# Optimization experiments

Measured on AMD Instinct MI355X. Metric: run time of the kernel, lower is better.

## Reference

```python
import jax, jax.numpy as jnp
import numpy as np

B = 2097152
SCALE, SHIFT = 1.5, 0.2
EPS = 1e-5
H, DK = 2, 2  # num_heads, d_k (embed_dim=4)


def _lin(x, w, b):
    return x @ w.T + b


def _ln(x, w, b):
    mu = jnp.mean(x, -1, keepdims=True)
    var = jnp.mean((x - mu) ** 2, -1, keepdims=True)
    return (x - mu) / jnp.sqrt(var + EPS) * w + b


def setup_inputs() -> dict:
    key = jax.random.key(0)
    ks = iter(jax.random.split(key, 40))
    def W(o, i):
        return jax.random.normal(next(ks), (o, i), jnp.float32) * (1.0 / np.sqrt(i))
    def Bv(o):
        return jax.random.normal(next(ks), (o,), jnp.float32) * 0.05
    d = {
        'inputs': jax.random.normal(next(ks), (B, 8), jnp.float32),
        'fm_w': W(16, 8), 'fm_b': Bv(16),
        'c1_w': W(16, 16), 'c1_b': Bv(16),
        'p1_w': W(12, 16), 'p1_b': Bv(12),
        'c2_w': W(8, 12), 'c2_b': Bv(8),
        'p2_w': W(4, 8), 'p2_b': Bv(4),
        'c3_w': W(4, 4), 'c3_b': Bv(4),
        'q_w': W(4, 4), 'q_b': Bv(4),
        'k_w': W(4, 4), 'k_b': Bv(4),
        'v_w': W(4, 4), 'v_b': Bv(4),
        'o_w': W(4, 4), 'o_b': Bv(4),
        'ln1_w': jnp.ones(4), 'ln1_b': jnp.zeros(4),
        'ln2_w': jnp.ones(4), 'ln2_b': jnp.zeros(4),
        'ffn1_w': W(8, 4), 'ffn1_b': Bv(8),
        'ffn2_w': W(4, 8), 'ffn2_b': Bv(4),
        'fs_w': W(4, 4), 'fs_b': Bv(4),
        'head_w': W(1, 4), 'head_b': Bv(1),
    }
    return d


def reference(inputs, fm_w, fm_b, c1_w, c1_b, p1_w, p1_b, c2_w, c2_b, p2_w, p2_b,
              c3_w, c3_b, q_w, q_b, k_w, k_b, v_w, v_b, o_w, o_b,
              ln1_w, ln1_b, ln2_w, ln2_b, ffn1_w, ffn1_b, ffn2_w, ffn2_b,
              fs_w, fs_b, head_w, head_b):
    x = jnp.tanh(_lin(inputs, fm_w, fm_b))
    x = jnp.tanh(_lin(x, c1_w, c1_b))
    x = jnp.tanh(_lin(x, p1_w, p1_b))
    x = jnp.tanh(_lin(x, c2_w, c2_b))
    x = jnp.tanh(_lin(x, p2_w, p2_b))
    x = jnp.tanh(_lin(x, c3_w, c3_b))
    # transformer block with seq_len = 1 (eval mode -> dropout identity)
    xs = x[:, None, :]  # [B, 1, 4]
    b, s, _ = xs.shape
    q = _lin(xs, q_w, q_b).reshape(b, s, H, DK).transpose(0, 2, 1, 3)
    k = _lin(xs, k_w, k_b).reshape(b, s, H, DK).transpose(0, 2, 1, 3)
    v = _lin(xs, v_w, v_b).reshape(b, s, H, DK).transpose(0, 2, 1, 3)
    scores = jnp.einsum('bhsd,bhtd->bhst', q, k) / np.sqrt(DK).astype(np.float32)
    attn = jax.nn.softmax(scores, axis=-1)
    out = jnp.einsum('bhst,bhtd->bhsd', attn, v).transpose(0, 2, 1, 3).reshape(b, s, H * DK)
    attn_out = _lin(out, o_w, o_b)
    xs = _ln(xs + attn_out, ln1_w, ln1_b)
    ffn = _lin(jax.nn.relu(_lin(xs, ffn1_w, ffn1_b)), ffn2_w, ffn2_b)
    xs = _ln(xs + ffn, ln2_w, ln2_b)
    x = xs[:, 0, :]
    x = jnp.tanh(_lin(x, fs_w, fs_b)) * SCALE + SHIFT
    return jax.nn.sigmoid(_lin(x, head_w, head_b))
```

## Files before the change

kernel.cpp:

```cpp
#include <hip/hip_runtime.h>

#define BS 256

typedef float f32x2 __attribute__((ext_vector_type(2)));

__device__ __forceinline__ f32x2 splat2(float v) {
  f32x2 r; r[0] = v; r[1] = v; return r;
}
__device__ __forceinline__ f32x2 pkfma(float w, f32x2 x, f32x2 a) {
  return __builtin_elementwise_fma(splat2(w), x, a);
}

__device__ __forceinline__ f32x2 fast_tanh2(f32x2 x) {
  f32x2 z = x * 2.8853900817779268f;
  f32x2 t;
  t[0] = __builtin_amdgcn_exp2f(z[0]);
  t[1] = __builtin_amdgcn_exp2f(z[1]);
  f32x2 tp1 = t + 1.0f;
  f32x2 r;
  r[0] = __builtin_amdgcn_rcpf(tp1[0]);
  r[1] = __builtin_amdgcn_rcpf(tp1[1]);
  return __builtin_elementwise_fma(splat2(-2.0f), r, splat2(1.0f));
}
__device__ __forceinline__ f32x2 fast_sigmoid2(f32x2 x) {
  f32x2 z = x * -1.4426950408889634f;
  f32x2 t;
  t[0] = __builtin_amdgcn_exp2f(z[0]);
  t[1] = __builtin_amdgcn_exp2f(z[1]);
  f32x2 tp1 = t + 1.0f;
  f32x2 r;
  r[0] = __builtin_amdgcn_rcpf(tp1[0]);
  r[1] = __builtin_amdgcn_rcpf(tp1[1]);
  return r;
}
__device__ __forceinline__ f32x2 relu2(f32x2 x) {
  f32x2 r;
  r[0] = fmaxf(x[0], 0.0f);
  r[1] = fmaxf(x[1], 0.0f);
  return r;
}

#define D4(W, B, O, p0, p1, p2, p3)                                            \
  pkfma((W)[(O)*4 + 0], p0,                                                    \
  pkfma((W)[(O)*4 + 1], p1,                                                    \
  pkfma((W)[(O)*4 + 2], p2,                                                    \
  pkfma((W)[(O)*4 + 3], p3, splat2((B)[O])))))

#define D8(W, B, O, p0, p1, p2, p3, p4, p5, p6, p7)                            \
  pkfma((W)[(O)*8 + 0], p0,                                                    \
  pkfma((W)[(O)*8 + 1], p1,                                                    \
  pkfma((W)[(O)*8 + 2], p2,                                                    \
  pkfma((W)[(O)*8 + 3], p3,                                                    \
  pkfma((W)[(O)*8 + 4], p4,                                                    \
  pkfma((W)[(O)*8 + 5], p5,                                                    \
  pkfma((W)[(O)*8 + 6], p6,                                                    \
  pkfma((W)[(O)*8 + 7], p7, splat2((B)[O])))))))))

#define D12(W, B, O, p0, p1, p2, p3, p4, p5, p6, p7, p8, p9, pa, pb)           \
  pkfma((W)[(O)*12 + 0], p0,                                                   \
  pkfma((W)[(O)*12 + 1], p1,                                                   \
  pkfma((W)[(O)*12 + 2], p2,                                                   \
  pkfma((W)[(O)*12 + 3], p3,                                                   \
  pkfma((W)[(O)*12 + 4], p4,                                                   \
  pkfma((W)[(O)*12 + 5], p5,                                                   \
  pkfma((W)[(O)*12 + 6], p6,                                                   \
  pkfma((W)[(O)*12 + 7], p7,                                                   \
  pkfma((W)[(O)*12 + 8], p8,                                                   \
  pkfma((W)[(O)*12 + 9], p9,                                                   \
  pkfma((W)[(O)*12 +10], pa,                                                   \
  pkfma((W)[(O)*12 +11], pb, splat2((B)[O])))))))))))))

#define D16(W, B, O, p0, p1, p2, p3, p4, p5, p6, p7, p8, p9, pa, pb, pc, pd, pe, pf) \
  pkfma((W)[(O)*16 + 0], p0,                                                   \
  pkfma((W)[(O)*16 + 1], p1,                                                   \
  pkfma((W)[(O)*16 + 2], p2,                                                   \
  pkfma((W)[(O)*16 + 3], p3,                                                   \
  pkfma((W)[(O)*16 + 4], p4,                                                   \
  pkfma((W)[(O)*16 + 5], p5,                                                   \
  pkfma((W)[(O)*16 + 6], p6,                                                   \
  pkfma((W)[(O)*16 + 7], p7,                                                   \
  pkfma((W)[(O)*16 + 8], p8,                                                   \
  pkfma((W)[(O)*16 + 9], p9,                                                   \
  pkfma((W)[(O)*16 +10], pa,                                                   \
  pkfma((W)[(O)*16 +11], pb,                                                   \
  pkfma((W)[(O)*16 +12], pc,                                                   \
  pkfma((W)[(O)*16 +13], pd,                                                   \
  pkfma((W)[(O)*16 +14], pe,                                                   \
  pkfma((W)[(O)*16 +15], pf, splat2((B)[O])))))))))))))))))

__global__ void __launch_bounds__(BS) qcnn_pk2(
    const float* __restrict__ inp,
    const float* __restrict__ fm_w,  const float* __restrict__ fm_b,
    const float* __restrict__ c1_w,  const float* __restrict__ c1_b,
    const float* __restrict__ p1_w,  const float* __restrict__ p1_b,
    const float* __restrict__ c2_w,  const float* __restrict__ c2_b,
    const float* __restrict__ p2_w,  const float* __restrict__ p2_b,
    const float* __restrict__ c3_w,  const float* __restrict__ c3_b,
    const float* __restrict__ v_w,   const float* __restrict__ v_b,
    const float* __restrict__ o_w,   const float* __restrict__ o_b,
    const float* __restrict__ ln1_w, const float* __restrict__ ln1_b,
    const float* __restrict__ ln2_w, const float* __restrict__ ln2_b,
    const float* __restrict__ ffn1_w, const float* __restrict__ ffn1_b,
    const float* __restrict__ ffn2_w, const float* __restrict__ ffn2_b,
    const float* __restrict__ fs_w,  const float* __restrict__ fs_b,
    const float* __restrict__ head_w, const float* __restrict__ head_b,
    float* __restrict__ out, long long nrows) {
  const long long gid = (long long)blockIdx.x * BS + threadIdx.x;
  const long long row0 = gid * 2;
  if (row0 >= nrows) return;
  const bool ok1 = (row0 + 1) < nrows;

  const float4* __restrict__ in4 = reinterpret_cast<const float4*>(inp);
  float4 r0lo = in4[gid * 4 + 0];
  float4 r0hi = in4[gid * 4 + 1];
  float4 r1lo, r1hi;
  if (ok1) {
    r1lo = in4[gid * 4 + 2];
    r1hi = in4[gid * 4 + 3];
  } else {
    r1lo = float4{0.f, 0.f, 0.f, 0.f};
    r1hi = float4{0.f, 0.f, 0.f, 0.f};
  }
  f32x2 x0 = {r0lo.x, r1lo.x}, x1 = {r0lo.y, r1lo.y};
  f32x2 x2 = {r0lo.z, r1lo.z}, x3 = {r0lo.w, r1lo.w};
  f32x2 x4 = {r0hi.x, r1hi.x}, x5 = {r0hi.y, r1hi.y};
  f32x2 x6 = {r0hi.z, r1hi.z}, x7 = {r0hi.w, r1hi.w};

#define LFM(O) fast_tanh2(D8(fm_w, fm_b, O, x0, x1, x2, x3, x4, x5, x6, x7))
  f32x2 a0 = LFM(0),  a1 = LFM(1),  a2 = LFM(2),  a3 = LFM(3);
  f32x2 a4 = LFM(4),  a5 = LFM(5),  a6 = LFM(6),  a7 = LFM(7);
  f32x2 a8 = LFM(8),  a9 = LFM(9),  aa = LFM(10), ab = LFM(11);
  f32x2 ac = LFM(12), ad = LFM(13), ae = LFM(14), af = LFM(15);

#define LC1(O) fast_tanh2(D16(c1_w, c1_b, O, a0,a1,a2,a3,a4,a5,a6,a7,a8,a9,aa,ab,ac,ad,ae,af))
  f32x2 b0 = LC1(0),  b1 = LC1(1),  b2 = LC1(2),  b3 = LC1(3);
  f32x2 b4 = LC1(4),  b5 = LC1(5),  b6 = LC1(6),  b7 = LC1(7);
  f32x2 b8 = LC1(8),  b9 = LC1(9),  ba = LC1(10), bb = LC1(11);
  f32x2 bc = LC1(12), bd = LC1(13), be = LC1(14), bf = LC1(15);

#define LP1(O) fast_tanh2(D16(p1_w, p1_b, O, b0,b1,b2,b3,b4,b5,b6,b7,b8,b9,ba,bb,bc,bd,be,bf))
  f32x2 c0 = LP1(0),  c1 = LP1(1),  c2 = LP1(2),  c3 = LP1(3);
  f32x2 c4 = LP1(4),  c5 = LP1(5),  c6 = LP1(6),  c7 = LP1(7);
  f32x2 c8 = LP1(8),  c9 = LP1(9),  ca = LP1(10), cb = LP1(11);

#define LC2(O) fast_tanh2(D12(c2_w, c2_b, O, c0,c1,c2,c3,c4,c5,c6,c7,c8,c9,ca,cb))
  f32x2 d0 = LC2(0), d1 = LC2(1), d2 = LC2(2), d3 = LC2(3);
  f32x2 d4 = LC2(4), d5 = LC2(5), d6 = LC2(6), d7 = LC2(7);

#define LP2(O) fast_tanh2(D8(p2_w, p2_b, O, d0, d1, d2, d3, d4, d5, d6, d7))
  f32x2 e0 = LP2(0), e1 = LP2(1), e2 = LP2(2), e3 = LP2(3);

  f32x2 s0 = fast_tanh2(D4(c3_w, c3_b, 0, e0, e1, e2, e3));
  f32x2 s1 = fast_tanh2(D4(c3_w, c3_b, 1, e0, e1, e2, e3));
  f32x2 s2 = fast_tanh2(D4(c3_w, c3_b, 2, e0, e1, e2, e3));
  f32x2 s3 = fast_tanh2(D4(c3_w, c3_b, 3, e0, e1, e2, e3));

  f32x2 v0 = D4(v_w, v_b, 0, s0, s1, s2, s3);
  f32x2 v1 = D4(v_w, v_b, 1, s0, s1, s2, s3);
  f32x2 v2 = D4(v_w, v_b, 2, s0, s1, s2, s3);
  f32x2 v3 = D4(v_w, v_b, 3, s0, s1, s2, s3);
  f32x2 o0 = D4(o_w, o_b, 0, v0, v1, v2, v3);
  f32x2 o1 = D4(o_w, o_b, 1, v0, v1, v2, v3);
  f32x2 o2 = D4(o_w, o_b, 2, v0, v1, v2, v3);
  f32x2 o3 = D4(o_w, o_b, 3, v0, v1, v2, v3);

  f32x2 t0 = s0 + o0, t1 = s1 + o1, t2 = s2 + o2, t3 = s3 + o3;
  f32x2 mu = (t0 + t1 + t2 + t3) * 0.25f;
  f32x2 q0 = t0 - mu, q1 = t1 - mu, q2 = t2 - mu, q3 = t3 - mu;
  f32x2 var = (q0 * q0 + q1 * q1 + q2 * q2 + q3 * q3) * 0.25f + 1e-5f;
  f32x2 inv;
  inv[0] = __builtin_amdgcn_rsqf(var[0]);
  inv[1] = __builtin_amdgcn_rsqf(var[1]);
  f32x2 n0 = q0 * inv * ln1_w[0] + ln1_b[0];
  f32x2 n1 = q1 * inv * ln1_w[1] + ln1_b[1];
  f32x2 n2 = q2 * inv * ln1_w[2] + ln1_b[2];
  f32x2 n3 = q3 * inv * ln1_w[3] + ln1_b[3];

#define LF1(O) relu2(D4(ffn1_w, ffn1_b, O, n0, n1, n2, n3))
  f32x2 f0 = LF1(0), f1 = LF1(1), f2 = LF1(2), f3 = LF1(3);
  f32x2 f4 = LF1(4), f5 = LF1(5), f6 = LF1(6), f7 = LF1(7);
  f32x2 g0 = D8(ffn2_w, ffn2_b, 0, f0, f1, f2, f3, f4, f5, f6, f7);
  f32x2 g1 = D8(ffn2_w, ffn2_b, 1, f0, f1, f2, f3, f4, f5, f6, f7);
  f32x2 g2 = D8(ffn2_w, ffn2_b, 2, f0, f1, f2, f3, f4, f5, f6, f7);
  f32x2 g3 = D8(ffn2_w, ffn2_b, 3, f0, f1, f2, f3, f4, f5, f6, f7);

  f32x2 u0 = n0 + g0, u1 = n1 + g1, u2 = n2 + g2, u3 = n3 + g3;
  f32x2 mu2 = (u0 + u1 + u2 + u3) * 0.25f;
  f32x2 w0 = u0 - mu2, w1 = u1 - mu2, w2 = u2 - mu2, w3 = u3 - mu2;
  f32x2 var2 = (w0 * w0 + w1 * w1 + w2 * w2 + w3 * w3) * 0.25f + 1e-5f;
  f32x2 inv2;
  inv2[0] = __builtin_amdgcn_rsqf(var2[0]);
  inv2[1] = __builtin_amdgcn_rsqf(var2[1]);
  f32x2 m0 = w0 * inv2 * ln2_w[0] + ln2_b[0];
  f32x2 m1 = w1 * inv2 * ln2_w[1] + ln2_b[1];
  f32x2 m2 = w2 * inv2 * ln2_w[2] + ln2_b[2];
  f32x2 m3 = w3 * inv2 * ln2_w[3] + ln2_b[3];

  f32x2 h0 = fast_tanh2(D4(fs_w, fs_b, 0, m0, m1, m2, m3)) * 1.5f + 0.2f;
  f32x2 h1 = fast_tanh2(D4(fs_w, fs_b, 1, m0, m1, m2, m3)) * 1.5f + 0.2f;
  f32x2 h2 = fast_tanh2(D4(fs_w, fs_b, 2, m0, m1, m2, m3)) * 1.5f + 0.2f;
  f32x2 h3 = fast_tanh2(D4(fs_w, fs_b, 3, m0, m1, m2, m3)) * 1.5f + 0.2f;
  f32x2 y = pkfma(head_w[3], h3,
            pkfma(head_w[2], h2,
            pkfma(head_w[1], h1,
            pkfma(head_w[0], h0, splat2(head_b[0])))));
  y = fast_sigmoid2(y);

  if (ok1) {
    reinterpret_cast<float2*>(out)[gid] = make_float2(y[0], y[1]);
  } else {
    out[row0] = y[0];
  }
}

extern "C" void kernel_launch(void* const* d_in, const int* in_sizes, int n_in,
                              void* d_out, int out_size, void* d_ws, size_t ws_size,
                              hipStream_t stream) {
  const float* inp = (const float*)d_in[0];
  long long nrows = (long long)in_sizes[0] / 8;
  long long nthreads = (nrows + 1) / 2;
  dim3 grid((unsigned)((nthreads + BS - 1) / BS)), block(BS);
  qcnn_pk2<<<grid, block, 0, stream>>>(
      inp,
      (const float*)d_in[1],  (const float*)d_in[2],
      (const float*)d_in[3],  (const float*)d_in[4],
      (const float*)d_in[5],  (const float*)d_in[6],
      (const float*)d_in[7],  (const float*)d_in[8],
      (const float*)d_in[9],  (const float*)d_in[10],
      (const float*)d_in[11], (const float*)d_in[12],
      (const float*)d_in[17], (const float*)d_in[18],
      (const float*)d_in[19], (const float*)d_in[20],
      (const float*)d_in[21], (const float*)d_in[22],
      (const float*)d_in[23], (const float*)d_in[24],
      (const float*)d_in[25], (const float*)d_in[26],
      (const float*)d_in[27], (const float*)d_in[28],
      (const float*)d_in[29], (const float*)d_in[30],
      (const float*)d_in[31], (const float*)d_in[32],
      (float*)d_out, nrows);
}
```

Baseline: 59.44 us.

## Replace exp/rcp tanh with Pade rational and process four rows per thread

Swaps the transcendental-unit tanh (exp2 plus rcp) for a clamped [7/6] Pade rational approximation whose reciprocal is computed by a magic-constant guess refined with Newton steps, so the work runs entirely as packed FMA-able VALU ops. Each thread now handles four rows instead of two, giving more packed-math parallelism and float4 output stores. The cost is more ALU instructions per tanh, higher register pressure from the wider vectors, and half as many threads, which may reduce occupancy and latency hiding.

```diff
diff --git a/kernel.cpp b/kernel.cpp
--- a/kernel.cpp
+++ b/kernel.cpp
@@ -2,49 +2,62 @@
 
 #define BS 256
 
-typedef float f32x2 __attribute__((ext_vector_type(2)));
-
-__device__ __forceinline__ f32x2 splat2(float v) {
-  f32x2 r; r[0] = v; r[1] = v; return r;
-}
-__device__ __forceinline__ f32x2 pkfma(float w, f32x2 x, f32x2 a) {
-  return __builtin_elementwise_fma(splat2(w), x, a);
-}
-
-__device__ __forceinline__ f32x2 fast_tanh2(f32x2 x) {
-  f32x2 z = x * 2.8853900817779268f;
-  f32x2 t;
-  t[0] = __builtin_amdgcn_exp2f(z[0]);
-  t[1] = __builtin_amdgcn_exp2f(z[1]);
-  f32x2 tp1 = t + 1.0f;
-  f32x2 r;
-  r[0] = __builtin_amdgcn_rcpf(tp1[0]);
-  r[1] = __builtin_amdgcn_rcpf(tp1[1]);
-  return __builtin_elementwise_fma(splat2(-2.0f), r, splat2(1.0f));
-}
-__device__ __forceinline__ f32x2 fast_sigmoid2(f32x2 x) {
-  f32x2 z = x * -1.4426950408889634f;
-  f32x2 t;
-  t[0] = __builtin_amdgcn_exp2f(z[0]);
-  t[1] = __builtin_amdgcn_exp2f(z[1]);
-  f32x2 tp1 = t + 1.0f;
-  f32x2 r;
-  r[0] = __builtin_amdgcn_rcpf(tp1[0]);
-  r[1] = __builtin_amdgcn_rcpf(tp1[1]);
+typedef float f32x4 __attribute__((ext_vector_type(4)));
+typedef unsigned int u32x4 __attribute__((ext_vector_type(4)));
+
+__device__ __forceinline__ f32x4 splat4(float v) {
+  f32x4 r; r[0] = v; r[1] = v; r[2] = v; r[3] = v; return r;
+}
+__device__ __forceinline__ f32x4 pkfma(float w, f32x4 x, f32x4 a) {
+  return __builtin_elementwise_fma(splat4(w), x, a);
+}
+
+__device__ __forceinline__ f32x4 tanh_pade(f32x4 x) {
+  f32x4 a;
+#pragma unroll
+  for (int e = 0; e < 4; ++e) a[e] = __builtin_amdgcn_fmed3f(x[e], -6.0f, 6.0f);
+  f32x4 t = a * a;
+  f32x4 n = t + 378.0f;
+  n = __builtin_elementwise_fma(n, t, splat4(17325.0f));
+  n = __builtin_elementwise_fma(n, t, splat4(135135.0f));
+  n = n * a;
+  f32x4 d = __builtin_elementwise_fma(t, splat4(28.0f), splat4(3150.0f));
+  d = __builtin_elementwise_fma(d, t, splat4(62370.0f));
+  d = __builtin_elementwise_fma(d, t, splat4(135135.0f));
+  u32x4 bi = __builtin_bit_cast(u32x4, d);
+  u32x4 yi = 0x7EF311C3u - bi;
+  f32x4 y = __builtin_bit_cast(f32x4, yi);
+#pragma unroll
+  for (int it = 0; it < 3; ++it) {
+    f32x4 u = __builtin_elementwise_fma(-d, y, splat4(2.0f));
+    y = y * u;
+  }
+  f32x4 r = n * y;
+#pragma unroll
+  for (int e = 0; e < 4; ++e) r[e] = __builtin_amdgcn_fmed3f(r[e], -1.0f, 1.0f);
   return r;
 }
-__device__ __forceinline__ f32x2 relu2(f32x2 x) {
-  f32x2 r;
-  r[0] = fmaxf(x[0], 0.0f);
-  r[1] = fmaxf(x[1], 0.0f);
+
+__device__ __forceinline__ f32x4 fast_sigmoid4(f32x4 x) {
+  f32x4 z = x * -1.4426950408889634f;
+  f32x4 t;
+#pragma unroll
+  for (int e = 0; e < 4; ++e) t[e] = __builtin_amdgcn_exp2f(z[e]);
+  f32x4 tp1 = t + 1.0f;
+  f32x4 r;
+#pragma unroll
+  for (int e = 0; e < 4; ++e) r[e] = __builtin_amdgcn_rcpf(tp1[e]);
   return r;
+}
+__device__ __forceinline__ f32x4 relu4(f32x4 x) {
+  return __builtin_elementwise_max(x, splat4(0.0f));
 }
 
 #define D4(W, B, O, p0, p1, p2, p3)                                            \
   pkfma((W)[(O)*4 + 0], p0,                                                    \
   pkfma((W)[(O)*4 + 1], p1,                                                    \
   pkfma((W)[(O)*4 + 2], p2,                                                    \
-  pkfma((W)[(O)*4 + 3], p3, splat2((B)[O])))))
+  pkfma((W)[(O)*4 + 3], p3, splat4((B)[O])))))
 
 #define D8(W, B, O, p0, p1, p2, p3, p4, p5, p6, p7)                            \
   pkfma((W)[(O)*8 + 0], p0,                                                    \
@@ -54,7 +67,7 @@
   pkfma((W)[(O)*8 + 4], p4,                                                    \
   pkfma((W)[(O)*8 + 5], p5,                                                    \
   pkfma((W)[(O)*8 + 6], p6,                                                    \
-  pkfma((W)[(O)*8 + 7], p7, splat2((B)[O])))))))))
+  pkfma((W)[(O)*8 + 7], p7, splat4((B)[O])))))))))
 
 #define D12(W, B, O, p0, p1, p2, p3, p4, p5, p6, p7, p8, p9, pa, pb)           \
   pkfma((W)[(O)*12 + 0], p0,                                                   \
@@ -68,7 +81,7 @@
   pkfma((W)[(O)*12 + 8], p8,                                                   \
   pkfma((W)[(O)*12 + 9], p9,                                                   \
   pkfma((W)[(O)*12 +10], pa,                                                   \
-  pkfma((W)[(O)*12 +11], pb, splat2((B)[O])))))))))))))
+  pkfma((W)[(O)*12 +11], pb, splat4((B)[O])))))))))))))
 
 #define D16(W, B, O, p0, p1, p2, p3, p4, p5, p6, p7, p8, p9, pa, pb, pc, pd, pe, pf) \
   pkfma((W)[(O)*16 + 0], p0,                                                   \
@@ -86,9 +99,9 @@
   pkfma((W)[(O)*16 +12], pc,                                                   \
   pkfma((W)[(O)*16 +13], pd,                                                   \
   pkfma((W)[(O)*16 +14], pe,                                                   \
-  pkfma((W)[(O)*16 +15], pf, splat2((B)[O])))))))))))))))))
-
-__global__ void __launch_bounds__(BS) qcnn_pk2(
+  pkfma((W)[(O)*16 +15], pf, splat4((B)[O])))))))))))))))))
+
+__global__ void __launch_bounds__(BS) qcnn_pade(
     const float* __restrict__ inp,
     const float* __restrict__ fm_w,  const float* __restrict__ fm_b,
     const float* __restrict__ c1_w,  const float* __restrict__ c1_b,
@@ -106,110 +119,114 @@
     const float* __restrict__ head_w, const float* __restrict__ head_b,
     float* __restrict__ out, long long nrows) {
   const long long gid = (long long)blockIdx.x * BS + threadIdx.x;
-  const long long row0 = gid * 2;
+  const long long row0 = gid * 4;
   if (row0 >= nrows) return;
-  const bool ok1 = (row0 + 1) < nrows;
+  const long long rA = row0;
+  const long long rB = (row0 + 1 < nrows) ? row0 + 1 : nrows - 1;
+  const long long rC = (row0 + 2 < nrows) ? row0 + 2 : nrows - 1;
+  const long long rD = (row0 + 3 < nrows) ? row0 + 3 : nrows - 1;
 
   const float4* __restrict__ in4 = reinterpret_cast<const float4*>(inp);
-  float4 r0lo = in4[gid * 4 + 0];
-  float4 r0hi = in4[gid * 4 + 1];
-  float4 r1lo, r1hi;
-  if (ok1) {
-    r1lo = in4[gid * 4 + 2];
-    r1hi = in4[gid * 4 + 3];
-  } else {
-    r1lo = float4{0.f, 0.f, 0.f, 0.f};
-    r1hi = float4{0.f, 0.f, 0.f, 0.f};
-  }
-  f32x2 x0 = {r0lo.x, r1lo.x}, x1 = {r0lo.y, r1lo.y};
-  f32x2 x2 = {r0lo.z, r1lo.z}, x3 = {r0lo.w, r1lo.w};
-  f32x2 x4 = {r0hi.x, r1hi.x}, x5 = {r0hi.y, r1hi.y};
-  f32x2 x6 = {r0hi.z, r1hi.z}, x7 = {r0hi.w, r1hi.w};
-
-#define LFM(O) fast_tanh2(D8(fm_w, fm_b, O, x0, x1, x2, x3, x4, x5, x6, x7))
-  f32x2 a0 = LFM(0),  a1 = LFM(1),  a2 = LFM(2),  a3 = LFM(3);
-  f32x2 a4 = LFM(4),  a5 = LFM(5),  a6 = LFM(6),  a7 = LFM(7);
-  f32x2 a8 = LFM(8),  a9 = LFM(9),  aa = LFM(10), ab = LFM(11);
-  f32x2 ac = LFM(12), ad = LFM(13), ae = LFM(14), af = LFM(15);
-
-#define LC1(O) fast_tanh2(D16(c1_w, c1_b, O, a0,a1,a2,a3,a4,a5,a6,a7,a8,a9,aa,ab,ac,ad,ae,af))
-  f32x2 b0 = LC1(0),  b1 = LC1(1),  b2 = LC1(2),  b3 = LC1(3);
-  f32x2 b4 = LC1(4),  b5 = LC1(5),  b6 = LC1(6),  b7 = LC1(7);
-  f32x2 b8 = LC1(8),  b9 = LC1(9),  ba = LC1(10), bb = LC1(11);
-  f32x2 bc = LC1(12), bd = LC1(13), be = LC1(14), bf = LC1(15);
-
-#define LP1(O) fast_tanh2(D16(p1_w, p1_b, O, b0,b1,b2,b3,b4,b5,b6,b7,b8,b9,ba,bb,bc,bd,be,bf))
-  f32x2 c0 = LP1(0),  c1 = LP1(1),  c2 = LP1(2),  c3 = LP1(3);
-  f32x2 c4 = LP1(4),  c5 = LP1(5),  c6 = LP1(6),  c7 = LP1(7);
-  f32x2 c8 = LP1(8),  c9 = LP1(9),  ca = LP1(10), cb = LP1(11);
-
-#define LC2(O) fast_tanh2(D12(c2_w, c2_b, O, c0,c1,c2,c3,c4,c5,c6,c7,c8,c9,ca,cb))
-  f32x2 d0 = LC2(0), d1 = LC2(1), d2 = LC2(2), d3 = LC2(3);
-  f32x2 d4 = LC2(4), d5 = LC2(5), d6 = LC2(6), d7 = LC2(7);
-
-#define LP2(O) fast_tanh2(D8(p2_w, p2_b, O, d0, d1, d2, d3, d4, d5, d6, d7))
-  f32x2 e0 = LP2(0), e1 = LP2(1), e2 = LP2(2), e3 = LP2(3);
-
-  f32x2 s0 = fast_tanh2(D4(c3_w, c3_b, 0, e0, e1, e2, e3));
-  f32x2 s1 = fast_tanh2(D4(c3_w, c3_b, 1, e0, e1, e2, e3));
-  f32x2 s2 = fast_tanh2(D4(c3_w, c3_b, 2, e0, e1, e2, e3));
-  f32x2 s3 = fast_tanh2(D4(c3_w, c3_b, 3, e0, e1, e2, e3));
-
-  f32x2 v0 = D4(v_w, v_b, 0, s0, s1, s2, s3);
-  f32x2 v1 = D4(v_w, v_b, 1, s0, s1, s2, s3);
-  f32x2 v2 = D4(v_w, v_b, 2, s0, s1, s2, s3);
-  f32x2 v3 = D4(v_w, v_b, 3, s0, s1, s2, s3);
-  f32x2 o0 = D4(o_w, o_b, 0, v0, v1, v2, v3);
-  f32x2 o1 = D4(o_w, o_b, 1, v0, v1, v2, v3);
-  f32x2 o2 = D4(o_w, o_b, 2, v0, v1, v2, v3);
-  f32x2 o3 = D4(o_w, o_b, 3, v0, v1, v2, v3);
-
-  f32x2 t0 = s0 + o0, t1 = s1 + o1, t2 = s2 + o2, t3 = s3 + o3;
-  f32x2 mu = (t0 + t1 + t2 + t3) * 0.25f;
-  f32x2 q0 = t0 - mu, q1 = t1 - mu, q2 = t2 - mu, q3 = t3 - mu;
-  f32x2 var = (q0 * q0 + q1 * q1 + q2 * q2 + q3 * q3) * 0.25f + 1e-5f;
-  f32x2 inv;
-  inv[0] = __builtin_amdgcn_rsqf(var[0]);
-  inv[1] = __builtin_amdgcn_rsqf(var[1]);
-  f32x2 n0 = q0 * inv * ln1_w[0] + ln1_b[0];
-  f32x2 n1 = q1 * inv * ln1_w[1] + ln1_b[1];
-  f32x2 n2 = q2 * inv * ln1_w[2] + ln1_b[2];
-  f32x2 n3 = q3 * inv * ln1_w[3] + ln1_b[3];
-
-#define LF1(O) relu2(D4(ffn1_w, ffn1_b, O, n0, n1, n2, n3))
-  f32x2 f0 = LF1(0), f1 = LF1(1), f2 = LF1(2), f3 = LF1(3);
-  f32x2 f4 = LF1(4), f5 = LF1(5), f6 = LF1(6), f7 = LF1(7);
-  f32x2 g0 = D8(ffn2_w, ffn2_b, 0, f0, f1, f2, f3, f4, f5, f6, f7);
-  f32x2 g1 = D8(ffn2_w, ffn2_b, 1, f0, f1, f2, f3, f4, f5, f6, f7);
-  f32x2 g2 = D8(ffn2_w, ffn2_b, 2, f0, f1, f2, f3, f4, f5, f6, f7);
-  f32x2 g3 = D8(ffn2_w, ffn2_b, 3, f0, f1, f2, f3, f4, f5, f6, f7);
-
-  f32x2 u0 = n0 + g0, u1 = n1 + g1, u2 = n2 + g2, u3 = n3 + g3;
-  f32x2 mu2 = (u0 + u1 + u2 + u3) * 0.25f;
-  f32x2 w0 = u0 - mu2, w1 = u1 - mu2, w2 = u2 - mu2, w3 = u3 - mu2;
-  f32x2 var2 = (w0 * w0 + w1 * w1 + w2 * w2 + w3 * w3) * 0.25f + 1e-5f;
-  f32x2 inv2;
-  inv2[0] = __builtin_amdgcn_rsqf(var2[0]);
-  inv2[1] = __builtin_amdgcn_rsqf(var2[1]);
-  f32x2 m0 = w0 * inv2 * ln2_w[0] + ln2_b[0];
-  f32x2 m1 = w1 * inv2 * ln2_w[1] + ln2_b[1];
-  f32x2 m2 = w2 * inv2 * ln2_w[2] + ln2_b[2];
-  f32x2 m3 = w3 * inv2 * ln2_w[3] + ln2_b[3];
-
-  f32x2 h0 = fast_tanh2(D4(fs_w, fs_b, 0, m0, m1, m2, m3)) * 1.5f + 0.2f;
-  f32x2 h1 = fast_tanh2(D4(fs_w, fs_b, 1, m0, m1, m2, m3)) * 1.5f + 0.2f;
-  f32x2 h2 = fast_tanh2(D4(fs_w, fs_b, 2, m0, m1, m2, m3)) * 1.5f + 0.2f;
-  f32x2 h3 = fast_tanh2(D4(fs_w, fs_b, 3, m0, m1, m2, m3)) * 1.5f + 0.2f;
-  f32x2 y = pkfma(head_w[3], h3,
+  float4 aLo = in4[rA * 2 + 0], aHi = in4[rA * 2 + 1];
+  float4 bLo = in4[rB * 2 + 0], bHi = in4[rB * 2 + 1];
+  float4 cLo = in4[rC * 2 + 0], cHi = in4[rC * 2 + 1];
+  float4 dLo = in4[rD * 2 + 0], dHi = in4[rD * 2 + 1];
+  f32x4 x0 = {aLo.x, bLo.x, cLo.x, dLo.x};
+  f32x4 x1 = {aLo.y, bLo.y, cLo.y, dLo.y};
+  f32x4 x2 = {aLo.z, bLo.z, cLo.z, dLo.z};
+  f32x4 x3 = {aLo.w, bLo.w, cLo.w, dLo.w};
+  f32x4 x4 = {aHi.x, bHi.x, cHi.x, dHi.x};
+  f32x4 x5 = {aHi.y, bHi.y, cHi.y, dHi.y};
+  f32x4 x6 = {aHi.z, bHi.z, cHi.z, dHi.z};
+  f32x4 x7 = {aHi.w, bHi.w, cHi.w, dHi.w};
+
+#define LFM(O) tanh_pade(D8(fm_w, fm_b, O, x0, x1, x2, x3, x4, x5, x6, x7))
+  f32x4 a0 = LFM(0),  a1 = LFM(1),  a2 = LFM(2),  a3 = LFM(3);
+  f32x4 a4 = LFM(4),  a5 = LFM(5),  a6 = LFM(6),  a7 = LFM(7);
+  f32x4 a8 = LFM(8),  a9 = LFM(9),  aa = LFM(10), ab = LFM(11);
+  f32x4 ac = LFM(12), ad = LFM(13), ae = LFM(14), af = LFM(15);
+
+#define LC1(O) tanh_pade(D16(c1_w, c1_b, O, a0,a1,a2,a3,a4,a5,a6,a7,a8,a9,aa,ab,ac,ad,ae,af))
+  f32x4 b0 = LC1(0),  b1 = LC1(1),  b2 = LC1(2),  b3 = LC1(3);
+  f32x4 b4 = LC1(4),  b5 = LC1(5),  b6 = LC1(6),  b7 = LC1(7);
+  f32x4 b8 = LC1(8),  b9 = LC1(9),  ba = LC1(10), bb = LC1(11);
+  f32x4 bc = LC1(12), bd = LC1(13), be = LC1(14), bf = LC1(15);
+
+#define LP1(O) tanh_pade(D16(p1_w, p1_b, O, b0,b1,b2,b3,b4,b5,b6,b7,b8,b9,ba,bb,bc,bd,be,bf))
+  f32x4 c0 = LP1(0),  c1 = LP1(1),  c2 = LP1(2),  c3 = LP1(3);
+  f32x4 c4 = LP1(4),  c5 = LP1(5),  c6 = LP1(6),  c7 = LP1(7);
+  f32x4 c8 = LP1(8),  c9 = LP1(9),  ca = LP1(10), cb = LP1(11);
+
+#define LC2(O) tanh_pade(D12(c2_w, c2_b, O, c0,c1,c2,c3,c4,c5,c6,c7,c8,c9,ca,cb))
+  f32x4 d0 = LC2(0), d1 = LC2(1), d2 = LC2(2), d3 = LC2(3);
+  f32x4 d4 = LC2(4), d5 = LC2(5), d6 = LC2(6), d7 = LC2(7);
+
+#define LP2(O) tanh_pade(D8(p2_w, p2_b, O, d0, d1, d2, d3, d4, d5, d6, d7))
+  f32x4 e0 = LP2(0), e1 = LP2(1), e2 = LP2(2), e3 = LP2(3);
+
+  f32x4 s0 = tanh_pade(D4(c3_w, c3_b, 0, e0, e1, e2, e3));
+  f32x4 s1 = tanh_pade(D4(c3_w, c3_b, 1, e0, e1, e2, e3));
+  f32x4 s2 = tanh_pade(D4(c3_w, c3_b, 2, e0, e1, e2, e3));
+  f32x4 s3 = tanh_pade(D4(c3_w, c3_b, 3, e0, e1, e2, e3));
+
+  f32x4 v0 = D4(v_w, v_b, 0, s0, s1, s2, s3);
+  f32x4 v1 = D4(v_w, v_b, 1, s0, s1, s2, s3);
+  f32x4 v2 = D4(v_w, v_b, 2, s0, s1, s2, s3);
+  f32x4 v3 = D4(v_w, v_b, 3, s0, s1, s2, s3);
+  f32x4 o0 = D4(o_w, o_b, 0, v0, v1, v2, v3);
+  f32x4 o1 = D4(o_w, o_b, 1, v0, v1, v2, v3);
+  f32x4 o2 = D4(o_w, o_b, 2, v0, v1, v2, v3);
+  f32x4 o3 = D4(o_w, o_b, 3, v0, v1, v2, v3);
+
+  f32x4 t0 = s0 + o0, t1 = s1 + o1, t2 = s2 + o2, t3 = s3 + o3;
+  f32x4 mu = (t0 + t1 + t2 + t3) * 0.25f;
+  f32x4 q0 = t0 - mu, q1 = t1 - mu, q2 = t2 - mu, q3 = t3 - mu;
+  f32x4 var = (q0 * q0 + q1 * q1 + q2 * q2 + q3 * q3) * 0.25f + 1e-5f;
+  f32x4 inv;
+#pragma unroll
+  for (int e = 0; e < 4; ++e) inv[e] = __builtin_amdgcn_rsqf(var[e]);
+  f32x4 n0 = q0 * inv * ln1_w[0] + ln1_b[0];
+  f32x4 n1 = q1 * inv * ln1_w[1] + ln1_b[1];
+  f32x4 n2 = q2 * inv * ln1_w[2] + ln1_b[2];
+  f32x4 n3 = q3 * inv * ln1_w[3] + ln1_b[3];
+
+#define LF1(O) relu4(D4(ffn1_w, ffn1_b, O, n0, n1, n2, n3))
+  f32x4 f0 = LF1(0), f1 = LF1(1), f2 = LF1(2), f3 = LF1(3);
+  f32x4 f4 = LF1(4), f5 = LF1(5), f6 = LF1(6), f7 = LF1(7);
+  f32x4 g0 = D8(ffn2_w, ffn2_b, 0, f0, f1, f2, f3, f4, f5, f6, f7);
+  f32x4 g1 = D8(ffn2_w, ffn2_b, 1, f0, f1, f2, f3, f4, f5, f6, f7);
+  f32x4 g2 = D8(ffn2_w, ffn2_b, 2, f0, f1, f2, f3, f4, f5, f6, f7);
+  f32x4 g3 = D8(ffn2_w, ffn2_b, 3, f0, f1, f2, f3, f4, f5, f6, f7);
+
+  f32x4 u0 = n0 + g0, u1 = n1 + g1, u2 = n2 + g2, u3 = n3 + g3;
+  f32x4 mu2 = (u0 + u1 + u2 + u3) * 0.25f;
+  f32x4 w0 = u0 - mu2, w1 = u1 - mu2, w2 = u2 - mu2, w3 = u3 - mu2;
+  f32x4 var2 = (w0 * w0 + w1 * w1 + w2 * w2 + w3 * w3) * 0.25f + 1e-5f;
+  f32x4 inv2;
+#pragma unroll
+  for (int e = 0; e < 4; ++e) inv2[e] = __builtin_amdgcn_rsqf(var2[e]);
+  f32x4 m0 = w0 * inv2 * ln2_w[0] + ln2_b[0];
+  f32x4 m1 = w1 * inv2 * ln2_w[1] + ln2_b[1];
+  f32x4 m2 = w2 * inv2 * ln2_w[2] + ln2_b[2];
+  f32x4 m3 = w3 * inv2 * ln2_w[3] + ln2_b[3];
+
+  f32x4 h0 = tanh_pade(D4(fs_w, fs_b, 0, m0, m1, m2, m3)) * 1.5f + 0.2f;
+  f32x4 h1 = tanh_pade(D4(fs_w, fs_b, 1, m0, m1, m2, m3)) * 1.5f + 0.2f;
+  f32x4 h2 = tanh_pade(D4(fs_w, fs_b, 2, m0, m1, m2, m3)) * 1.5f + 0.2f;
+  f32x4 h3 = tanh_pade(D4(fs_w, fs_b, 3, m0, m1, m2, m3)) * 1.5f + 0.2f;
+  f32x4 y = pkfma(head_w[3], h3,
             pkfma(head_w[2], h2,
             pkfma(head_w[1], h1,
-            pkfma(head_w[0], h0, splat2(head_b[0])))));
-  y = fast_sigmoid2(y);
-
-  if (ok1) {
-    reinterpret_cast<float2*>(out)[gid] = make_float2(y[0], y[1]);
+            pkfma(head_w[0], h0, splat4(head_b[0])))));
+  y = fast_sigmoid4(y);
+
+  if (row0 + 3 < nrows) {
+    reinterpret_cast<float4*>(out)[gid] = float4{y[0], y[1], y[2], y[3]};
   } else {
-    out[row0] = y[0];
+    out[rA] = y[0];
+    if (rB > rA) out[rB] = y[1];
+    if (rC > rB) out[rC] = y[2];
+    if (rD > rC) out[rD] = y[3];
   }
 }
 
@@ -218,9 +235,9 @@
                               hipStream_t stream) {
   const float* inp = (const float*)d_in[0];
   long long nrows = (long long)in_sizes[0] / 8;
-  long long nthreads = (nrows + 1) / 2;
+  long long nthreads = (nrows + 3) / 4;
   dim3 grid((unsigned)((nthreads + BS - 1) / BS)), block(BS);
-  qcnn_pk2<<<grid, block, 0, stream>>>(
+  qcnn_pade<<<grid, block, 0, stream>>>(
       inp,
       (const float*)d_in[1],  (const float*)d_in[2],
       (const float*)d_in[3],  (const float*)d_in[4],
```

After: 80.25 us. +35.0%, slower.
